# Kernel optimization log

Measured on AMD Instinct MI355X. Metric: run time of the kernel, lower is better.

The kernel has to match this reference:

```python
import jax, jax.numpy as jnp
import numpy as np

N_NODES = 50000
N_EDGES = 800000
DIM = 128
N_LAYERS = 5
BN_EPS = 1e-5


def setup_inputs() -> dict:
    key = jax.random.key(0)
    ks = jax.random.split(key, 8)
    x = jax.random.normal(ks[0], (N_NODES, DIM), dtype=jnp.float32)
    edge_index = jax.random.randint(ks[1], (2, N_EDGES), 0, N_NODES, dtype=jnp.int64)
    batch = jnp.sort(jax.random.randint(ks[2], (N_NODES,), 0, 64, dtype=jnp.int64))
    scale = 1.0 / np.sqrt(DIM)
    W1 = jax.random.normal(ks[3], (N_LAYERS, DIM, DIM), dtype=jnp.float32) * scale
    b1 = jnp.zeros((N_LAYERS, DIM), dtype=jnp.float32)
    W2 = jax.random.normal(ks[4], (N_LAYERS, DIM, DIM), dtype=jnp.float32) * scale
    b2 = jnp.zeros((N_LAYERS, DIM), dtype=jnp.float32)
    gamma = jnp.ones((N_LAYERS, DIM), dtype=jnp.float32)
    beta = jnp.zeros((N_LAYERS, DIM), dtype=jnp.float32)
    return {"x": x, "edge_index": edge_index, "batch": batch,
            "W1": W1, "b1": b1, "W2": W2, "b2": b2,
            "gamma": gamma, "beta": beta}


def _gin_layer(x, src, dst, w1, bb1, w2, bb2, g, b):
    # GINConv (eps=0): h_i = MLP(x_i + sum_{j->i} x_j)
    agg = jax.ops.segment_sum(x[src], dst, num_segments=N_NODES)  # [N, D]
    h = x + agg
    h = jnp.maximum(h @ w1 + bb1, 0.0) @ w2 + bb2  # 2-layer MLP
    h = jnp.maximum(h, 0.0)                        # outer ReLU
    # BatchNorm1d (training-mode batch stats, biased variance)
    mu = jnp.mean(h, axis=0)
    var = jnp.mean(jnp.square(h - mu), axis=0)
    return (h - mu) * jax.lax.rsqrt(var + BN_EPS) * g + b


def reference(x, edge_index, batch, W1, b1, W2, b2, gamma, beta):
    src, dst = edge_index[0], edge_index[1]
    xs = []
    h = x
    for i in range(N_LAYERS):
        h = _gin_layer(h, src, dst, W1[i], b1[i], W2[i], b2[i], gamma[i], beta[i])
        xs.append(h)
    return h, jnp.stack(xs)
```

## Files before the change

kernel.cpp:

```cpp
#include <hip/hip_runtime.h>

#define N_NODES 50000
#define DIM 128
#define N_LAYERS 5
#define BN_EPS 1e-5f

typedef __attribute__((ext_vector_type(8))) short short8;
typedef __attribute__((ext_vector_type(4))) float f32x4;

__device__ __forceinline__ float bf2f(unsigned int u16) {
    union { unsigned int i; float f; } c; c.i = u16 << 16; return c.f;
}
__device__ __forceinline__ unsigned short f2bf(float f) {
    union { float f; unsigned int i; } c; c.f = f;
    unsigned int v = c.i + 0x7FFFu + ((c.i >> 16) & 1u);
    return (unsigned short)(v >> 16);
}


__global__ void hist_kernel(const int* __restrict__ dst, int n_edges, int* __restrict__ counts) {
    int e = blockIdx.x * 256 + threadIdx.x;
    if (e < n_edges) atomicAdd(&counts[dst[e]], 1);
}

__global__ void scan_local(const int* __restrict__ counts, int n,
                           int* __restrict__ offsets, int* __restrict__ blocksums) {
    __shared__ int temp[256];
    int t = threadIdx.x;
    int i = blockIdx.x * 256 + t;
    int v = (i < n) ? counts[i] : 0;
    temp[t] = v;
    __syncthreads();
    for (int off = 1; off < 256; off <<= 1) {
        int add = (t >= off) ? temp[t - off] : 0;
        __syncthreads();
        temp[t] += add;
        __syncthreads();
    }
    if (i < n) offsets[i] = temp[t] - v;
    if (t == 255) blocksums[blockIdx.x] = temp[255];
}

__global__ void scan_block(int* __restrict__ blocksums, int nb) {
    __shared__ int temp[256];
    int t = threadIdx.x;
    int v = (t < nb) ? blocksums[t] : 0;
    temp[t] = v;
    __syncthreads();
    for (int off = 1; off < 256; off <<= 1) {
        int add = (t >= off) ? temp[t - off] : 0;
        __syncthreads();
        temp[t] += add;
        __syncthreads();
    }
    if (t < nb) blocksums[t] = temp[t] - v;
}

__global__ void scan_add(int* __restrict__ offsets, int* __restrict__ cursor,
                         const int* __restrict__ blocksums, int n, int n_edges) {
    int i = blockIdx.x * 256 + threadIdx.x;
    if (i < n) {
        int val = offsets[i] + blocksums[blockIdx.x];
        offsets[i] = val;
        cursor[i] = val;
    }
    if (i == 0) offsets[n] = n_edges;
}

__global__ void scatter_kernel(const int* __restrict__ src, const int* __restrict__ dst,
                               int n_edges, int* __restrict__ cursor, int* __restrict__ csr_src) {
    int e = blockIdx.x * 256 + threadIdx.x;
    if (e < n_edges) {
        int p = atomicAdd(&cursor[dst[e]], 1);
        csr_src[p] = src[e];
    }
}


__global__ void wpack_prep(const float* __restrict__ W1, const float* __restrict__ W2,
                           unsigned short* __restrict__ wp) {
    int idx = blockIdx.x * 256 + threadIdx.x;
    if (idx >= N_LAYERS * 2 * 16384) return;
    int j    = idx & 7;
    int lane = (idx >> 3) & 63;
    int nt   = (idx >> 9) & 7;
    int ks   = (idx >> 12) & 3;
    int mat  = (idx >> 14) & 1;
    int lay  = idx >> 15;
    int l15 = lane & 15, l4 = lane >> 4;
    int col = nt * 16 + l15;
    int kp = ks * 32 + l4 * 8 + j;
    int k = mat ? ((kp & 7) * 16 + (kp >> 3)) : kp;
    const float* W = mat ? W2 : W1;
    float w = W[((size_t)lay * 128 + k) * 128 + col];
    unsigned short hi = f2bf(w);
    unsigned short lo = f2bf(w - bf2f(hi));
    size_t base = (size_t)(lay * 2 + mat) * 32768;
    size_t inner = (size_t)((ks * 8 + nt) * 64 + lane) * 8 + j;
    wp[base + inner] = hi;
    wp[base + 16384 + inner] = lo;
}


__global__ void agg_kernel(const float* __restrict__ x, const int* __restrict__ csr_src,
                           const int* __restrict__ offsets,
                           unsigned int* __restrict__ h_hi_u, unsigned int* __restrict__ h_lo_u) {
    int wave = threadIdx.x >> 6;
    int l = threadIdx.x & 63;
    int node = blockIdx.x * 4 + wave;
    if (node >= N_NODES) return;
    int half = l >> 5;
    int d4 = l & 31;
    int beg = offsets[node], end = offsets[node + 1];
    const float4* x4 = (const float4*)x;

    float4 acc = make_float4(0.f, 0.f, 0.f, 0.f);
    if (half == 0) acc = x4[(size_t)node * 32 + d4];

    for (int e = beg; e < end; e += 16) {
        int s[8];
#pragma unroll
        for (int i = 0; i < 8; ++i) s[i] = csr_src[min(e + 2 * i + half, end - 1)];
        float4 v[8];
#pragma unroll
        for (int i = 0; i < 8; ++i) v[i] = x4[(size_t)s[i] * 32 + d4];
#pragma unroll
        for (int i = 0; i < 8; ++i) {
            float w = (e + 2 * i + half < end) ? 1.0f : 0.0f;
            acc.x = fmaf(v[i].x, w, acc.x);
            acc.y = fmaf(v[i].y, w, acc.y);
            acc.z = fmaf(v[i].z, w, acc.z);
            acc.w = fmaf(v[i].w, w, acc.w);
        }
    }

    acc.x += __shfl_xor(acc.x, 32);
    acc.y += __shfl_xor(acc.y, 32);
    acc.z += __shfl_xor(acc.z, 32);
    acc.w += __shfl_xor(acc.w, 32);

    unsigned short h0 = f2bf(acc.x), h1 = f2bf(acc.y);
    unsigned short h2 = f2bf(acc.z), h3 = f2bf(acc.w);
    if (half == 0) {
        uint2 hv;
        hv.x = (unsigned int)h0 | ((unsigned int)h1 << 16);
        hv.y = (unsigned int)h2 | ((unsigned int)h3 << 16);
        ((uint2*)h_hi_u)[(size_t)node * 32 + d4] = hv;
    } else {
        unsigned short l0 = f2bf(acc.x - bf2f(h0)), l1 = f2bf(acc.y - bf2f(h1));
        unsigned short l2 = f2bf(acc.z - bf2f(h2)), l3 = f2bf(acc.w - bf2f(h3));
        uint2 lv;
        lv.x = (unsigned int)l0 | ((unsigned int)l1 << 16);
        lv.y = (unsigned int)l2 | ((unsigned int)l3 << 16);
        ((uint2*)h_lo_u)[(size_t)node * 32 + d4] = lv;
    }
}

__global__ void agg_bf_kernel(const uint2* __restrict__ xbf2, const int* __restrict__ csr_src,
                              const int* __restrict__ offsets,
                              unsigned int* __restrict__ h_hi_u, unsigned int* __restrict__ h_lo_u) {
    int wave = threadIdx.x >> 6;
    int l = threadIdx.x & 63;
    int node = blockIdx.x * 4 + wave;
    if (node >= N_NODES) return;
    int half = l >> 5;
    int d = l & 31;
    int beg = offsets[node], end = offsets[node + 1];

    float a0 = 0.f, a1 = 0.f, a2 = 0.f, a3 = 0.f;
    if (half == 0) {
        uint2 u = xbf2[(size_t)node * 32 + d];
        a0 = bf2f(u.x & 0xFFFFu); a1 = bf2f(u.x >> 16);
        a2 = bf2f(u.y & 0xFFFFu); a3 = bf2f(u.y >> 16);
    }

    for (int e = beg; e < end; e += 16) {
        int s[8];
#pragma unroll
        for (int i = 0; i < 8; ++i) s[i] = csr_src[min(e + 2 * i + half, end - 1)];
        uint2 v[8];
#pragma unroll
        for (int i = 0; i < 8; ++i) v[i] = xbf2[(size_t)s[i] * 32 + d];
#pragma unroll
        for (int i = 0; i < 8; ++i) {
            float w = (e + 2 * i + half < end) ? 1.0f : 0.0f;
            a0 = fmaf(bf2f(v[i].x & 0xFFFFu), w, a0);
            a1 = fmaf(bf2f(v[i].x >> 16),     w, a1);
            a2 = fmaf(bf2f(v[i].y & 0xFFFFu), w, a2);
            a3 = fmaf(bf2f(v[i].y >> 16),     w, a3);
        }
    }

    a0 += __shfl_xor(a0, 32);
    a1 += __shfl_xor(a1, 32);
    a2 += __shfl_xor(a2, 32);
    a3 += __shfl_xor(a3, 32);

    unsigned short h0 = f2bf(a0), h1 = f2bf(a1), h2 = f2bf(a2), h3 = f2bf(a3);
    if (half == 0) {
        uint2 hv;
        hv.x = (unsigned int)h0 | ((unsigned int)h1 << 16);
        hv.y = (unsigned int)h2 | ((unsigned int)h3 << 16);
        ((uint2*)h_hi_u)[(size_t)node * 32 + d] = hv;
    } else {
        unsigned short l0 = f2bf(a0 - bf2f(h0)), l1 = f2bf(a1 - bf2f(h1));
        unsigned short l2 = f2bf(a2 - bf2f(h2)), l3 = f2bf(a3 - bf2f(h3));
        uint2 lv;
        lv.x = (unsigned int)l0 | ((unsigned int)l1 << 16);
        lv.y = (unsigned int)l2 | ((unsigned int)l3 << 16);
        ((uint2*)h_lo_u)[(size_t)node * 32 + d] = lv;
    }
}

__global__ __launch_bounds__(128) void mlp_mfma(
        const unsigned short* __restrict__ h_hi, const unsigned short* __restrict__ h_lo,
        const short8* __restrict__ wp1, const float* __restrict__ b1,
        const short8* __restrict__ wp2, const float* __restrict__ b2,
        float* __restrict__ h_raw,
        float* __restrict__ part_s, float* __restrict__ part_q) {
    __shared__ unsigned short mid_hi[2][2][16][128];
    __shared__ unsigned short mid_lo[2][2][16][128];
    __shared__ float red_s[2][128], red_q[2][128];
    int t = threadIdx.x, wave = t >> 6, l = t & 63;
    int l15 = l & 15, l4 = l >> 4;
    int row_base = blockIdx.x * 64 + wave * 32;

    int r0 = row_base + l15, r1 = r0 + 16;
    int cr0 = min(r0, N_NODES - 1), cr1 = min(r1, N_NODES - 1);
    const short8* ah0p = (const short8*)(h_hi + (size_t)cr0 * 128);
    const short8* ah1p = (const short8*)(h_hi + (size_t)cr1 * 128);
    const short8* al0p = (const short8*)(h_lo + (size_t)cr0 * 128);
    const short8* al1p = (const short8*)(h_lo + (size_t)cr1 * 128);

    const short8* wp1l = wp1 + 2048;
    const short8* wp2l = wp2 + 2048;

    f32x4 acc[2][8];
#pragma unroll
    for (int m = 0; m < 2; ++m)
#pragma unroll
        for (int nt = 0; nt < 8; ++nt) acc[m][nt] = (f32x4)0.0f;

#pragma unroll
    for (int ks = 0; ks < 4; ++ks) {
        short8 ah0 = ah0p[ks * 4 + l4];
        short8 ah1 = ah1p[ks * 4 + l4];
        short8 al0 = al0p[ks * 4 + l4];
        short8 al1 = al1p[ks * 4 + l4];
#pragma unroll
        for (int nt = 0; nt < 8; ++nt) {
            short8 whi = wp1[(ks * 8 + nt) * 64 + l];
            short8 wlo = wp1l[(ks * 8 + nt) * 64 + l];
            acc[0][nt] = __builtin_amdgcn_mfma_f32_16x16x32_bf16(ah0, whi, acc[0][nt], 0, 0, 0);
            acc[0][nt] = __builtin_amdgcn_mfma_f32_16x16x32_bf16(al0, whi, acc[0][nt], 0, 0, 0);
            acc[0][nt] = __builtin_amdgcn_mfma_f32_16x16x32_bf16(ah0, wlo, acc[0][nt], 0, 0, 0);
            acc[1][nt] = __builtin_amdgcn_mfma_f32_16x16x32_bf16(ah1, whi, acc[1][nt], 0, 0, 0);
            acc[1][nt] = __builtin_amdgcn_mfma_f32_16x16x32_bf16(al1, whi, acc[1][nt], 0, 0, 0);
            acc[1][nt] = __builtin_amdgcn_mfma_f32_16x16x32_bf16(ah1, wlo, acc[1][nt], 0, 0, 0);
        }
    }

    float b1v[8];
#pragma unroll
    for (int nt = 0; nt < 8; ++nt) b1v[nt] = b1[nt * 16 + l15];

#pragma unroll
    for (int m = 0; m < 2; ++m) {
#pragma unroll
        for (int rr = 0; rr < 4; ++rr) {
            int row = l4 * 4 + rr;
            short8 ph, pl;
#pragma unroll
            for (int nt = 0; nt < 8; ++nt) {
                float v = fmaxf(acc[m][nt][rr] + b1v[nt], 0.0f);
                unsigned short hv = f2bf(v);
                ph[nt] = (short)hv;
                pl[nt] = (short)f2bf(v - bf2f(hv));
            }
            int off = (l15 * 16) ^ ((row & 7) << 4);
            *(short8*)((char*)&mid_hi[wave][m][row][0] + off) = ph;
            *(short8*)((char*)&mid_lo[wave][m][row][0] + off) = pl;
        }
    }
    __syncthreads();

    f32x4 acc2[2][8];
#pragma unroll
    for (int m = 0; m < 2; ++m)
#pragma unroll
        for (int nt = 0; nt < 8; ++nt) acc2[m][nt] = (f32x4)0.0f;

#pragma unroll
    for (int ks = 0; ks < 4; ++ks) {
        int off = (ks * 64 + l4 * 16) ^ ((l15 & 7) << 4);
        short8 ah0 = *(const short8*)((char*)&mid_hi[wave][0][l15][0] + off);
        short8 ah1 = *(const short8*)((char*)&mid_hi[wave][1][l15][0] + off);
        short8 al0 = *(const short8*)((char*)&mid_lo[wave][0][l15][0] + off);
        short8 al1 = *(const short8*)((char*)&mid_lo[wave][1][l15][0] + off);
#pragma unroll
        for (int nt = 0; nt < 8; ++nt) {
            short8 whi = wp2[(ks * 8 + nt) * 64 + l];
            short8 wlo = wp2l[(ks * 8 + nt) * 64 + l];
            acc2[0][nt] = __builtin_amdgcn_mfma_f32_16x16x32_bf16(ah0, whi, acc2[0][nt], 0, 0, 0);
            acc2[0][nt] = __builtin_amdgcn_mfma_f32_16x16x32_bf16(al0, whi, acc2[0][nt], 0, 0, 0);
            acc2[0][nt] = __builtin_amdgcn_mfma_f32_16x16x32_bf16(ah0, wlo, acc2[0][nt], 0, 0, 0);
            acc2[1][nt] = __builtin_amdgcn_mfma_f32_16x16x32_bf16(ah1, whi, acc2[1][nt], 0, 0, 0);
            acc2[1][nt] = __builtin_amdgcn_mfma_f32_16x16x32_bf16(al1, whi, acc2[1][nt], 0, 0, 0);
            acc2[1][nt] = __builtin_amdgcn_mfma_f32_16x16x32_bf16(ah1, wlo, acc2[1][nt], 0, 0, 0);
        }
    }

    float b2v[8];
#pragma unroll
    for (int nt = 0; nt < 8; ++nt) b2v[nt] = b2[nt * 16 + l15];

    float s[8], q[8];
#pragma unroll
    for (int nt = 0; nt < 8; ++nt) { s[nt] = 0.0f; q[nt] = 0.0f; }

#pragma unroll
    for (int m = 0; m < 2; ++m) {
#pragma unroll
        for (int rr = 0; rr < 4; ++rr) {
            int rg = row_base + m * 16 + l4 * 4 + rr;
            bool ok = rg < N_NODES;
#pragma unroll
            for (int nt = 0; nt < 8; ++nt) {
                float v = fmaxf(acc2[m][nt][rr] + b2v[nt], 0.0f);
                if (ok) {
                    h_raw[(size_t)rg * 128 + nt * 16 + l15] = v;
                    s[nt] += v;
                    q[nt] += v * v;
                }
            }
        }
    }
#pragma unroll
    for (int nt = 0; nt < 8; ++nt) {
        s[nt] += __shfl_xor(s[nt], 16); s[nt] += __shfl_xor(s[nt], 32);
        q[nt] += __shfl_xor(q[nt], 16); q[nt] += __shfl_xor(q[nt], 32);
    }
    if (l4 == 0) {
#pragma unroll
        for (int nt = 0; nt < 8; ++nt) {
            red_s[wave][nt * 16 + l15] = s[nt];
            red_q[wave][nt * 16 + l15] = q[nt];
        }
    }
    __syncthreads();
    if (t < 128) {
        part_s[blockIdx.x * 128 + t] = red_s[0][t] + red_s[1][t];
        part_q[blockIdx.x * 128 + t] = red_q[0][t] + red_q[1][t];
    }
}

__global__ __launch_bounds__(256) void bn_reduce(
        const float* __restrict__ part_s, const float* __restrict__ part_q,
        float* __restrict__ bn_sum, float* __restrict__ bn_sq, int nparts) {
    __shared__ float red[256];
    int c = blockIdx.x & 127;
    const float* src = (blockIdx.x >> 7) ? part_q : part_s;
    float* dst = (blockIdx.x >> 7) ? bn_sq : bn_sum;
    float a = 0.0f;
    for (int p = threadIdx.x; p < nparts; p += 256) a += src[p * 128 + c];
    red[threadIdx.x] = a;
    __syncthreads();
    for (int s = 128; s > 0; s >>= 1) {
        if (threadIdx.x < s) red[threadIdx.x] += red[threadIdx.x + s];
        __syncthreads();
    }
    if (threadIdx.x == 0) dst[c] = red[0];
}

__global__ void bn_apply(float* __restrict__ h,
                         const float* __restrict__ bn_sum, const float* __restrict__ bn_sq,
                         const float* __restrict__ gamma, const float* __restrict__ beta,
                         uint2* __restrict__ xbf_next, float4* __restrict__ dup) {
    int i4 = blockIdx.x * 256 + threadIdx.x;
    if (i4 >= N_NODES * DIM / 4) return;
    float4 v = ((const float4*)h)[i4];
    int c0 = (i4 & 31) * 4;
    const float invN = 1.0f / (float)N_NODES;
    float* vp = (float*)&v;
#pragma unroll
    for (int j = 0; j < 4; ++j) {
        int c = c0 + j;
        float mean = bn_sum[c] * invN;
        float var = fmaxf(bn_sq[c] * invN - mean * mean, 0.0f);
        float inv = rsqrtf(var + BN_EPS);
        vp[j] = (vp[j] - mean) * inv * gamma[c] + beta[c];
    }
    ((float4*)h)[i4] = v;
    if (xbf_next) {
        unsigned int lo = (unsigned int)f2bf(vp[0]) | ((unsigned int)f2bf(vp[1]) << 16);
        unsigned int hi = (unsigned int)f2bf(vp[2]) | ((unsigned int)f2bf(vp[3]) << 16);
        xbf_next[i4] = make_uint2(lo, hi);
    }
    if (dup) dup[i4] = v;
}


extern "C" void kernel_launch(void* const* d_in, const int* in_sizes, int n_in,
                              void* d_out, int out_size, void* d_ws, size_t ws_size,
                              hipStream_t stream) {
    const float* x     = (const float*)d_in[0];
    const int*   eidx  = (const int*)d_in[1];
    const float* W1    = (const float*)d_in[3];
    const float* b1    = (const float*)d_in[4];
    const float* W2    = (const float*)d_in[5];
    const float* b2    = (const float*)d_in[6];
    const float* gamma = (const float*)d_in[7];
    const float* beta  = (const float*)d_in[8];

    int n_edges = in_sizes[1] / 2;
    const int* src = eidx;
    const int* dst = eidx + n_edges;

    const int NBLK = (N_NODES + 63) / 64;

    int* counts    = (int*)d_ws;
    int* offsets   = counts + N_NODES;
    int* cursor    = offsets + N_NODES + 1;
    int* blocksums = cursor + N_NODES;
    int* csr_src   = blocksums + 256;
    float* part_s  = (float*)(csr_src + n_edges);
    float* part_q  = part_s + NBLK * 128;
    float* bn_sum  = part_q + NBLK * 128;
    float* bn_sq   = bn_sum + DIM;
    size_t wp_off = (((size_t)(bn_sq + DIM) - (size_t)d_ws) + 15) & ~(size_t)15;
    unsigned short* wp = (unsigned short*)((char*)d_ws + wp_off);
    uint2* x_bf2 = (uint2*)(wp + (size_t)N_LAYERS * 2 * 32768);

    float* out = (float*)d_out;
    unsigned int* h_hi_u = (unsigned int*)d_out;
    unsigned int* h_lo_u = h_hi_u + (size_t)N_NODES * 64;
    const unsigned short* h_hi = (const unsigned short*)h_hi_u;
    const unsigned short* h_lo = (const unsigned short*)h_lo_u;

    hipMemsetAsync(counts, 0, N_NODES * sizeof(int), stream);
    hist_kernel<<<(n_edges + 255) / 256, 256, 0, stream>>>(dst, n_edges, counts);
    int nb = (N_NODES + 255) / 256;
    scan_local<<<nb, 256, 0, stream>>>(counts, N_NODES, offsets, blocksums);
    scan_block<<<1, 256, 0, stream>>>(blocksums, nb);
    scan_add<<<nb, 256, 0, stream>>>(offsets, cursor, blocksums, N_NODES, n_edges);
    scatter_kernel<<<(n_edges + 255) / 256, 256, 0, stream>>>(src, dst, n_edges, cursor, csr_src);

    wpack_prep<<<(N_LAYERS * 2 * 16384 + 255) / 256, 256, 0, stream>>>(W1, W2, wp);

    for (int i = 0; i < N_LAYERS; ++i) {
        float* layer_out = out + (size_t)(1 + i) * N_NODES * DIM;
        if (i == 0)
            agg_kernel<<<(N_NODES + 3) / 4, 256, 0, stream>>>(x, csr_src, offsets,
                                                              h_hi_u, h_lo_u);
        else
            agg_bf_kernel<<<(N_NODES + 3) / 4, 256, 0, stream>>>(x_bf2, csr_src, offsets,
                                                                 h_hi_u, h_lo_u);
        mlp_mfma<<<NBLK, 128, 0, stream>>>(
            h_hi, h_lo,
            (const short8*)(wp + (size_t)(i * 2) * 32768), b1 + (size_t)i * DIM,
            (const short8*)(wp + (size_t)(i * 2 + 1) * 32768), b2 + (size_t)i * DIM,
            layer_out, part_s, part_q);
        bn_reduce<<<256, 256, 0, stream>>>(part_s, part_q, bn_sum, bn_sq, NBLK);
        bn_apply<<<(N_NODES * DIM / 4 + 255) / 256, 256, 0, stream>>>(
            layer_out, bn_sum, bn_sq, gamma + (size_t)i * DIM, beta + (size_t)i * DIM,
            (i < N_LAYERS - 1) ? x_bf2 : (uint2*)nullptr,
            (i == N_LAYERS - 1) ? (float4*)out : (float4*)nullptr);
    }
}
```

Before: 531.3 us.

## Split neighbor aggregation into column-slice passes for cache-resident gathers

```diff
diff --git a/kernel.cpp b/kernel.cpp
--- a/kernel.cpp
+++ b/kernel.cpp
@@ -102,31 +102,31 @@
 }
 
 
-__global__ void agg_kernel(const float* __restrict__ x, const int* __restrict__ csr_src,
-                           const int* __restrict__ offsets,
-                           unsigned int* __restrict__ h_hi_u, unsigned int* __restrict__ h_lo_u) {
+__global__ void agg_pass_fp32(const float4* __restrict__ x4, const int* __restrict__ csr_src,
+                              const int* __restrict__ offsets, int pass,
+                              unsigned int* __restrict__ h_hi_u, unsigned int* __restrict__ h_lo_u) {
     int wave = threadIdx.x >> 6;
     int l = threadIdx.x & 63;
     int node = blockIdx.x * 4 + wave;
     if (node >= N_NODES) return;
-    int half = l >> 5;
-    int d4 = l & 31;
+    int g = l >> 3;
+    int d = l & 7;
+    int cbase = pass * 8 + d;
     int beg = offsets[node], end = offsets[node + 1];
-    const float4* x4 = (const float4*)x;
 
     float4 acc = make_float4(0.f, 0.f, 0.f, 0.f);
-    if (half == 0) acc = x4[(size_t)node * 32 + d4];
-
-    for (int e = beg; e < end; e += 16) {
+    if (g == 0) acc = x4[(size_t)node * 32 + cbase];
+
+    for (int e = beg; e < end; e += 64) {
         int s[8];
 #pragma unroll
-        for (int i = 0; i < 8; ++i) s[i] = csr_src[min(e + 2 * i + half, end - 1)];
+        for (int i = 0; i < 8; ++i) s[i] = csr_src[min(e + 8 * i + g, end - 1)];
         float4 v[8];
 #pragma unroll
-        for (int i = 0; i < 8; ++i) v[i] = x4[(size_t)s[i] * 32 + d4];
+        for (int i = 0; i < 8; ++i) v[i] = x4[(size_t)s[i] * 32 + cbase];
 #pragma unroll
         for (int i = 0; i < 8; ++i) {
-            float w = (e + 2 * i + half < end) ? 1.0f : 0.0f;
+            float w = (e + 8 * i + g < end) ? 1.0f : 0.0f;
             acc.x = fmaf(v[i].x, w, acc.x);
             acc.y = fmaf(v[i].y, w, acc.y);
             acc.z = fmaf(v[i].z, w, acc.z);
@@ -134,56 +134,59 @@
         }
     }
 
-    acc.x += __shfl_xor(acc.x, 32);
-    acc.y += __shfl_xor(acc.y, 32);
-    acc.z += __shfl_xor(acc.z, 32);
-    acc.w += __shfl_xor(acc.w, 32);
+    acc.x += __shfl_xor(acc.x, 8);  acc.y += __shfl_xor(acc.y, 8);
+    acc.z += __shfl_xor(acc.z, 8);  acc.w += __shfl_xor(acc.w, 8);
+    acc.x += __shfl_xor(acc.x, 16); acc.y += __shfl_xor(acc.y, 16);
+    acc.z += __shfl_xor(acc.z, 16); acc.w += __shfl_xor(acc.w, 16);
+    acc.x += __shfl_xor(acc.x, 32); acc.y += __shfl_xor(acc.y, 32);
+    acc.z += __shfl_xor(acc.z, 32); acc.w += __shfl_xor(acc.w, 32);
 
     unsigned short h0 = f2bf(acc.x), h1 = f2bf(acc.y);
     unsigned short h2 = f2bf(acc.z), h3 = f2bf(acc.w);
-    if (half == 0) {
+    if (g == 0) {
         uint2 hv;
         hv.x = (unsigned int)h0 | ((unsigned int)h1 << 16);
         hv.y = (unsigned int)h2 | ((unsigned int)h3 << 16);
-        ((uint2*)h_hi_u)[(size_t)node * 32 + d4] = hv;
-    } else {
+        ((uint2*)h_hi_u)[(size_t)node * 32 + cbase] = hv;
+    } else if (g == 1) {
         unsigned short l0 = f2bf(acc.x - bf2f(h0)), l1 = f2bf(acc.y - bf2f(h1));
         unsigned short l2 = f2bf(acc.z - bf2f(h2)), l3 = f2bf(acc.w - bf2f(h3));
         uint2 lv;
         lv.x = (unsigned int)l0 | ((unsigned int)l1 << 16);
         lv.y = (unsigned int)l2 | ((unsigned int)l3 << 16);
-        ((uint2*)h_lo_u)[(size_t)node * 32 + d4] = lv;
-    }
-}
-
-__global__ void agg_bf_kernel(const uint2* __restrict__ xbf2, const int* __restrict__ csr_src,
-                              const int* __restrict__ offsets,
-                              unsigned int* __restrict__ h_hi_u, unsigned int* __restrict__ h_lo_u) {
+        ((uint2*)h_lo_u)[(size_t)node * 32 + cbase] = lv;
+    }
+}
+
+__global__ void agg_pass_bf(const uint2* __restrict__ xb2, const int* __restrict__ csr_src,
+                            const int* __restrict__ offsets, int pass,
+                            unsigned int* __restrict__ h_hi_u, unsigned int* __restrict__ h_lo_u) {
     int wave = threadIdx.x >> 6;
     int l = threadIdx.x & 63;
     int node = blockIdx.x * 4 + wave;
     if (node >= N_NODES) return;
-    int half = l >> 5;
-    int d = l & 31;
+    int g = l >> 4;
+    int d = l & 15;
+    int cbase = pass * 16 + d;
     int beg = offsets[node], end = offsets[node + 1];
 
     float a0 = 0.f, a1 = 0.f, a2 = 0.f, a3 = 0.f;
-    if (half == 0) {
-        uint2 u = xbf2[(size_t)node * 32 + d];
+    if (g == 0) {
+        uint2 u = xb2[(size_t)node * 32 + cbase];
         a0 = bf2f(u.x & 0xFFFFu); a1 = bf2f(u.x >> 16);
         a2 = bf2f(u.y & 0xFFFFu); a3 = bf2f(u.y >> 16);
     }
 
-    for (int e = beg; e < end; e += 16) {
+    for (int e = beg; e < end; e += 32) {
         int s[8];
 #pragma unroll
-        for (int i = 0; i < 8; ++i) s[i] = csr_src[min(e + 2 * i + half, end - 1)];
+        for (int i = 0; i < 8; ++i) s[i] = csr_src[min(e + 4 * i + g, end - 1)];
         uint2 v[8];
 #pragma unroll
-        for (int i = 0; i < 8; ++i) v[i] = xbf2[(size_t)s[i] * 32 + d];
+        for (int i = 0; i < 8; ++i) v[i] = xb2[(size_t)s[i] * 32 + cbase];
 #pragma unroll
         for (int i = 0; i < 8; ++i) {
-            float w = (e + 2 * i + half < end) ? 1.0f : 0.0f;
+            float w = (e + 4 * i + g < end) ? 1.0f : 0.0f;
             a0 = fmaf(bf2f(v[i].x & 0xFFFFu), w, a0);
             a1 = fmaf(bf2f(v[i].x >> 16),     w, a1);
             a2 = fmaf(bf2f(v[i].y & 0xFFFFu), w, a2);
@@ -191,24 +194,24 @@
         }
     }
 
-    a0 += __shfl_xor(a0, 32);
-    a1 += __shfl_xor(a1, 32);
-    a2 += __shfl_xor(a2, 32);
-    a3 += __shfl_xor(a3, 32);
+    a0 += __shfl_xor(a0, 16); a1 += __shfl_xor(a1, 16);
+    a2 += __shfl_xor(a2, 16); a3 += __shfl_xor(a3, 16);
+    a0 += __shfl_xor(a0, 32); a1 += __shfl_xor(a1, 32);
+    a2 += __shfl_xor(a2, 32); a3 += __shfl_xor(a3, 32);
 
     unsigned short h0 = f2bf(a0), h1 = f2bf(a1), h2 = f2bf(a2), h3 = f2bf(a3);
-    if (half == 0) {
+    if (g == 0) {
         uint2 hv;
         hv.x = (unsigned int)h0 | ((unsigned int)h1 << 16);
         hv.y = (unsigned int)h2 | ((unsigned int)h3 << 16);
-        ((uint2*)h_hi_u)[(size_t)node * 32 + d] = hv;
-    } else {
+        ((uint2*)h_hi_u)[(size_t)node * 32 + cbase] = hv;
+    } else if (g == 1) {
         unsigned short l0 = f2bf(a0 - bf2f(h0)), l1 = f2bf(a1 - bf2f(h1));
         unsigned short l2 = f2bf(a2 - bf2f(h2)), l3 = f2bf(a3 - bf2f(h3));
         uint2 lv;
         lv.x = (unsigned int)l0 | ((unsigned int)l1 << 16);
         lv.y = (unsigned int)l2 | ((unsigned int)l3 << 16);
-        ((uint2*)h_lo_u)[(size_t)node * 32 + d] = lv;
+        ((uint2*)h_lo_u)[(size_t)node * 32 + cbase] = lv;
     }
 }
 
@@ -429,7 +432,8 @@
     float* bn_sq   = bn_sum + DIM;
     size_t wp_off = (((size_t)(bn_sq + DIM) - (size_t)d_ws) + 15) & ~(size_t)15;
     unsigned short* wp = (unsigned short*)((char*)d_ws + wp_off);
-    uint2* x_bf2 = (uint2*)(wp + (size_t)N_LAYERS * 2 * 32768);
+    size_t xb_off = (wp_off + (size_t)N_LAYERS * 2 * 32768 * 2 + 15) & ~(size_t)15;
+    uint2* x_bf2 = (uint2*)((char*)d_ws + xb_off);
 
     float* out = (float*)d_out;
     unsigned int* h_hi_u = (unsigned int*)d_out;
@@ -447,14 +451,18 @@
 
     wpack_prep<<<(N_LAYERS * 2 * 16384 + 255) / 256, 256, 0, stream>>>(W1, W2, wp);
 
+    const int AGG_BLKS = (N_NODES + 3) / 4;
     for (int i = 0; i < N_LAYERS; ++i) {
         float* layer_out = out + (size_t)(1 + i) * N_NODES * DIM;
-        if (i == 0)
-            agg_kernel<<<(N_NODES + 3) / 4, 256, 0, stream>>>(x, csr_src, offsets,
-                                                              h_hi_u, h_lo_u);
-        else
-            agg_bf_kernel<<<(N_NODES + 3) / 4, 256, 0, stream>>>(x_bf2, csr_src, offsets,
-                                                                 h_hi_u, h_lo_u);
+        if (i == 0) {
+            for (int p = 0; p < 4; ++p)
+                agg_pass_fp32<<<AGG_BLKS, 256, 0, stream>>>(
+                    (const float4*)x, csr_src, offsets, p, h_hi_u, h_lo_u);
+        } else {
+            for (int p = 0; p < 2; ++p)
+                agg_pass_bf<<<AGG_BLKS, 256, 0, stream>>>(
+                    x_bf2, csr_src, offsets, p, h_hi_u, h_lo_u);
+        }
         mlp_mfma<<<NBLK, 128, 0, stream>>>(
             h_hi, h_lo,
             (const short8*)(wp + (size_t)(i * 2) * 32768), b1 + (size_t)i * DIM,
```

Result: slower. 622.4 us (+17.1%).
